# Optimization experiments

Measured on AMD Instinct MI355X. Metric: run time of the kernel, lower is better.

The kernel has to match this reference:

```python
import jax, jax.numpy as jnp
import numpy as np

B = 64      # num graphs
NPG = 800   # nodes per graph
N = B * NPG
EPG = 6400  # edges per graph (avg degree 8)
APG = 64    # feasible actions per graph
H = 4       # attention heads
C = 64      # hidden channels per head
OUT = 128   # out_channels


def _gat_params(key, fin, h, c, concat):
    k1, k2, k3 = jax.random.split(key, 3)
    s = 1.0 / np.sqrt(fin)
    W = jax.random.uniform(k1, (fin, h * c), jnp.float32, -s, s)
    a_src = jax.random.uniform(k2, (h, c), jnp.float32, -s, s)
    a_dst = jax.random.uniform(k3, (h, c), jnp.float32, -s, s)
    b = jnp.zeros((h * c if concat else c,), jnp.float32)
    return W, a_src, a_dst, b


def _lin_params(key, fin, fout):
    k1, k2 = jax.random.split(key)
    s = 1.0 / np.sqrt(fin)
    W = jax.random.uniform(k1, (fin, fout), jnp.float32, -s, s)
    b = jax.random.uniform(k2, (fout,), jnp.float32, -s, s)
    return W, b


def setup_inputs() -> dict:
    key = jax.random.key(0)
    ks = list(jax.random.split(key, 24))
    x = jax.random.normal(ks[0], (N, 5), jnp.float32)
    offs = jnp.arange(B, dtype=jnp.int32) * NPG
    src = jax.random.randint(ks[1], (B, EPG), 0, NPG, jnp.int32) + offs[:, None]
    dst = jax.random.randint(ks[2], (B, EPG), 0, NPG, jnp.int32) + offs[:, None]
    edge_index = jnp.stack([src.reshape(-1), dst.reshape(-1)])
    batch = jnp.repeat(jnp.arange(B, dtype=jnp.int32), NPG)
    actions_idx = (jax.random.randint(ks[3], (B, APG, 2), 0, NPG, jnp.int32)
                   + offs[:, None, None]).reshape(-1, 2)
    tabu_label = (jax.random.uniform(ks[4], (B * APG, 1)) < 0.5).astype(jnp.float32)
    inp = dict(x=x, edge_index=edge_index, batch=batch,
               actions_idx=actions_idx, tabu_label=tabu_label)
    names = ['f1', 'f2', 'f3', 'b1', 'b2', 'b3']
    fins = [3, H * C, H * C, 3, H * C, H * C]
    hs = [H, H, 1, H, H, 1]
    cs = [C, C, OUT, C, C, OUT]
    concats = [True, True, False, True, True, False]
    for i, nm in enumerate(names):
        W, a_s, a_d, b = _gat_params(ks[5 + i], fins[i], hs[i], cs[i], concats[i])
        inp[nm + '_W'] = W; inp[nm + '_as'] = a_s; inp[nm + '_ad'] = a_d; inp[nm + '_b'] = b
    dims = [(8 * OUT + 1, 2 * OUT), (2 * OUT, 2 * OUT), (2 * OUT, 2 * OUT), (2 * OUT, 1)]
    for i, (fi, fo) in enumerate(dims):
        W, b = _lin_params(ks[12 + i], fi, fo)
        inp['p_W%d' % (i + 1)] = W; inp['p_b%d' % (i + 1)] = b
    return inp


def _gat(h, s, d, W, a_src, a_dst, bias, concat):
    # PyG GATConv: project, per-edge attention, softmax over target index, scatter-add
    n = h.shape[0]
    Hh, Cc = a_src.shape
    xp = (h @ W).reshape(n, Hh, Cc)                      # [N,H,C]
    al_s = (xp * a_src).sum(-1)                          # [N,H]
    al_d = (xp * a_dst).sum(-1)                          # [N,H]
    e = jax.nn.leaky_relu(al_s[s] + al_d[d], 0.2)        # [E,H]
    m = jax.ops.segment_max(e, d, num_segments=n)
    ex = jnp.exp(e - m[d])
    den = jax.ops.segment_sum(ex, d, num_segments=n)
    alpha = ex / (den[d] + 1e-16)
    out = jax.ops.segment_sum(xp[s] * alpha[..., None], d, num_segments=n)  # [N,H,C]
    out = out.reshape(n, Hh * Cc) if concat else out.mean(axis=1)
    return out + bias


def reference(x, edge_index, batch, actions_idx, tabu_label,
              f1_W, f1_as, f1_ad, f1_b, f2_W, f2_as, f2_ad, f2_b,
              f3_W, f3_as, f3_ad, f3_b, b1_W, b1_as, b1_ad, b1_b,
              b2_W, b2_as, b2_ad, b2_b, b3_W, b3_as, b3_ad, b3_b,
              p_W1, p_b1, p_W2, p_b2, p_W3, p_b3, p_W4, p_b4):
    n = x.shape[0]
    ar = jnp.arange(n, dtype=edge_index.dtype)
    ei = jnp.concatenate([edge_index, jnp.stack([ar, ar])], axis=1)  # add_self_loops
    src, dst = ei[0], ei[1]
    # forward branch (flow source_to_target)
    hf = x[:, jnp.array([0, 1, 3])]
    hf = jax.nn.elu(_gat(hf, src, dst, f1_W, f1_as, f1_ad, f1_b, True))
    hf = jax.nn.elu(_gat(hf, src, dst, f2_W, f2_as, f2_ad, f2_b, True))
    hf3 = _gat(hf, src, dst, f3_W, f3_as, f3_ad, f3_b, False)
    # backward branch (flow target_to_source == reversed edges)
    hb = x[:, jnp.array([0, 2, 4])]
    hb = jax.nn.elu(_gat(hb, dst, src, b1_W, b1_as, b1_ad, b1_b, True))
    hb = jax.nn.elu(_gat(hb, dst, src, b2_W, b2_as, b2_ad, b2_b, True))
    hb3 = _gat(hb, dst, src, b3_W, b3_as, b3_ad, b3_b, False)
    h_node = jnp.concatenate([hf3, hb3], axis=-1)        # [N, 2*OUT]
    counts = jax.ops.segment_sum(jnp.ones((n,), x.dtype), batch, num_segments=B)
    g_pool = jax.ops.segment_sum(h_node, batch, num_segments=B) / counts[:, None]
    node_h = jnp.concatenate([h_node, g_pool[batch]], axis=-1)  # [N, 4*OUT]
    action_h = jnp.concatenate([node_h[actions_idx[:, 0]],
                                node_h[actions_idx[:, 1]],
                                tabu_label], axis=-1)    # [A, 8*OUT+1]
    h = jnp.tanh(action_h @ p_W1 + p_b1)
    h = jnp.tanh(h @ p_W2 + p_b2)
    h = jnp.tanh(h @ p_W3 + p_b3)
    score = (h @ p_W4 + p_b4).reshape(B, APG)
    log_prob = jax.nn.log_softmax(score, axis=-1)        # [B, APG]
    entropy = -(jnp.exp(log_prob) * log_prob).sum(-1, keepdims=True)  # [B,1]
    return (log_prob, entropy)
```

## Files before the change

kernel.cpp:

```cpp
#include <hip/hip_runtime.h>
#include <hip/hip_bf16.h>
#include <math.h>

constexpr int NN  = 51200;
constexpr int EE  = 409600;
constexpr int BB  = 64;
constexpr int APG = 64;
constexpr int NPG = 800;
constexpr int SCAN_N = 2 * NN;
constexpr int NA = BB * APG;
constexpr int KF = 1056;

typedef __bf16 bf16x8 __attribute__((ext_vector_type(8)));
typedef float f32x4 __attribute__((ext_vector_type(4)));
typedef float f32x2 __attribute__((ext_vector_type(2)));
typedef __attribute__((address_space(1))) const void g_void;
typedef __attribute__((address_space(3))) void l_void;

__device__ __forceinline__ float leaky(float x) { return fmaxf(x, 0.2f * x); }
__device__ __forceinline__ float bflo(unsigned w) { return __uint_as_float(w << 16); }
__device__ __forceinline__ float bfhi(unsigned w) { return __uint_as_float(w & 0xffff0000u); }
__device__ __forceinline__ unsigned short f2b(float x) {
  __hip_bfloat16 h = __float2bfloat16(x);
  unsigned short u;
  __builtin_memcpy(&u, &h, 2);
  return u;
}
__device__ __forceinline__ unsigned pack2(float a, float b) {
  return (unsigned)f2b(a) | ((unsigned)f2b(b) << 16);
}

__global__ void count_kernel(const int* __restrict__ ei, int* cnt) {
  int e = blockIdx.x * blockDim.x + threadIdx.x;
  if (e >= EE) return;
  int s = ei[e], d = ei[EE + e];
  atomicAdd(&cnt[d], 1);
  atomicAdd(&cnt[NN + s], 1);
}

__global__ __launch_bounds__(256) void scan1_kernel(const int* __restrict__ cnt,
                                                    int* __restrict__ rp,
                                                    int* __restrict__ bsum) {
  __shared__ int wsum[4];
  int b = blockIdx.x, t = threadIdx.x;
  int base = b * 1024 + t * 4;
  int4 v = *(const int4*)(cnt + base);
  int s = v.x + v.y + v.z + v.w;
  int lane = t & 63, wv = t >> 6;
  int incl = s;
  for (int off = 1; off < 64; off <<= 1) {
    int u = __shfl_up(incl, off);
    if (lane >= off) incl += u;
  }
  if (lane == 63) wsum[wv] = incl;
  __syncthreads();
  int woff = 0;
  for (int i = 0; i < wv; i++) woff += wsum[i];
  int excl = woff + incl - s;
  rp[base] = excl;
  rp[base + 1] = excl + v.x;
  rp[base + 2] = excl + v.x + v.y;
  rp[base + 3] = excl + v.x + v.y + v.z;
  if (t == 255) bsum[b] = woff + incl;
}

__global__ void scan2_kernel(const int* __restrict__ bsum, int* __restrict__ boff,
                             int* __restrict__ rp) {
  __shared__ int w0;
  int t = threadIdx.x;
  int v = (t < 100) ? bsum[t] : 0;
  int lane = t & 63;
  int incl = v;
  for (int off = 1; off < 64; off <<= 1) {
    int u = __shfl_up(incl, off);
    if (lane >= off) incl += u;
  }
  if (t == 63) w0 = incl;
  __syncthreads();
  int excl = incl - v + ((t >= 64) ? w0 : 0);
  if (t < 100) boff[t] = excl;
  if (t == 99) rp[SCAN_N] = excl + v;
}

__global__ __launch_bounds__(256) void scan3_kernel(int* __restrict__ rp,
                                                    const int* __restrict__ boff) {
  int b = blockIdx.x;
  int off = boff[b];
  int i = b * 1024 + threadIdx.x * 4;
  int4 v = *(int4*)(rp + i);
  v.x += off; v.y += off; v.z += off; v.w += off;
  *(int4*)(rp + i) = v;
}

__global__ void fill_kernel(const int* __restrict__ ei, const int* __restrict__ rp,
                            int* pos, int* __restrict__ col) {
  int e = blockIdx.x * blockDim.x + threadIdx.x;
  if (e >= EE) return;
  int s = ei[e], d = ei[EE + e];
  int p = atomicAdd(&pos[d], 1);
  col[rp[d] + p] = s;
  int q = atomicAdd(&pos[NN + s], 1);
  col[rp[NN + s] + q] = d;
}

__global__ __launch_bounds__(256) void precomp_kernel(const float* __restrict__ Wf,
                                                      const float* __restrict__ Wb,
                                                      const float* __restrict__ asf,
                                                      const float* __restrict__ adf,
                                                      const float* __restrict__ asb,
                                                      const float* __restrict__ adb,
                                                      float* __restrict__ wa) {
  int wave = (blockIdx.x * blockDim.x + threadIdx.x) >> 6;
  int lane = threadIdx.x & 63;
  if (wave >= 48) return;
  int dir = wave / 24, sd = (wave / 12) % 2, h = (wave / 3) % 4, c = wave % 3;
  const float* W = dir ? Wb : Wf;
  const float* a = dir ? (sd ? adb : asb) : (sd ? adf : asf);
  float v = W[c * 256 + h * 64 + lane] * a[h * 64 + lane];
  for (int off = 1; off < 64; off <<= 1) v += __shfl_xor(v, off);
  if (lane == 0) wa[wave] = v;
}

__global__ __launch_bounds__(256) void lin1_kernel(const float* __restrict__ x,
                                                   const float* __restrict__ Wf,
                                                   const float* __restrict__ Wb,
                                                   const float* __restrict__ wa,
                                                   __hip_bfloat16* __restrict__ out,
                                                   float* __restrict__ al_s,
                                                   float* __restrict__ al_d) {
  int idx = blockIdx.x * 256 + threadIdx.x;
  int n = idx >> 5, grp = idx & 31;
  int dir = (n >= NN) ? 1 : 0;
  int node = dir ? n - NN : n;
  const float* W = dir ? Wb : Wf;
  int c1 = dir ? 2 : 1, c2 = dir ? 4 : 3;
  float f0 = x[node * 5], f1 = x[node * 5 + c1], f2 = x[node * 5 + c2];
  int j0 = grp * 8;
  float v[8];
#pragma unroll
  for (int j = 0; j < 8; j++)
    v[j] = f0 * W[j0 + j] + f1 * W[256 + j0 + j] + f2 * W[512 + j0 + j];
  uint4 u;
  u.x = pack2(v[0], v[1]);
  u.y = pack2(v[2], v[3]);
  u.z = pack2(v[4], v[5]);
  u.w = pack2(v[6], v[7]);
  *(uint4*)(out + (size_t)n * 256 + j0) = u;
  if (grp < 4) {
    const float* ws = wa + dir * 24 + grp * 3;
    const float* wd = wa + dir * 24 + 12 + grp * 3;
    al_s[n * 4 + grp] = f0 * ws[0] + f1 * ws[1] + f2 * ws[2];
    al_d[n * 4 + grp] = f0 * wd[0] + f1 * wd[1] + f2 * wd[2];
  }
}

__device__ __forceinline__ f32x2 unpk(unsigned w) {
  f32x2 v;
  v.x = bflo(w);
  v.y = bfhi(w);
  return v;
}

template <int HH, int CC, int OUT_SPLIT>
__global__ __launch_bounds__(256) void spmm_kernel(const __hip_bfloat16* __restrict__ xp,
                                                   const float* __restrict__ als,
                                                   const float* __restrict__ ald,
                                                   const int* __restrict__ rp,
                                                   const int* __restrict__ col,
                                                   const float* __restrict__ biasf,
                                                   const float* __restrict__ biasb,
                                                   __hip_bfloat16* __restrict__ out_bf,
                                                   int do_elu) {
  constexpr int HC = HH * CC;
  constexpr int RDW = HC / 2;
  constexpr int DL = RDW / 32;
  constexpr int NWQ = (HH == 4) ? 8 : 2;
  int b = blockIdx.x;
  int xcd = b & 7;
  int bq = b >> 3;
  int dreg = xcd * 12800;
  int t = threadIdx.x;
  int wv = t >> 6, lane = t & 63;
  int sub = lane & 31, halfsel = lane >> 5;
  int lbase = lane & 32;
  int off_row = (dreg >= NN) ? NN : 0;
  const float* bias = (dreg >= NN) ? biasb : biasf;
  int hch = (HH == 4) ? (sub >> 3) : 0;
  int hat = (HH == 4) ? (sub & 3) : 0;
  const unsigned* xw = (const unsigned*)xp;
  float bv[2 * DL];
#pragma unroll
  for (int j = 0; j < 2 * DL; j++) bv[j] = bias[sub * 2 * DL + j];

#pragma unroll 1
  for (int it = 0; it < 4; ++it) {
    int d = dreg + it * 3200 + bq * 8 + wv * 2 + halfsel;
    int beg = rp[d];
    int deg = rp[d + 1] - beg;
    int degmax = max(deg, __shfl_xor(deg, 32));
    degmax = __builtin_amdgcn_readfirstlane(degmax);

    float ald_d = ald[(size_t)d * HH + hat];
    float als_d = als[(size_t)d * HH + hat];
    float selfw = __expf(leaky(als_d + ald_d));

    int e0 = (sub < deg) ? sub : (deg - 1);
    e0 = (e0 < 0) ? 0 : e0;
    int cA = col[beg + e0];
    cA = (((unsigned)cA < (unsigned)NN) ? cA : 0) + off_row;
    int cB = off_row;
    if (degmax > 32) {
      int e1 = (32 + sub < deg) ? (32 + sub) : (deg - 1);
      e1 = (e1 < 0) ? 0 : e1;
      cB = col[beg + e1];
      cB = (((unsigned)cB < (unsigned)NN) ? cB : 0) + off_row;
    }

    float wq[NWQ];
    float den = 0.f;
    if constexpr (HH == 4) {
#pragma unroll
      for (int g = 0; g < 8; ++g) {
        float w = 0.f;
        if (g * 8 < degmax) {
          int e = g * 8 + (sub >> 2);
          int s = __shfl((g < 4) ? cA : cB, lbase + (g & 3) * 8 + (sub >> 2));
          if (e < deg) w = __expf(leaky(als[(size_t)s * 4 + hat] + ald_d));
        }
        wq[g] = w;
        den += w;
      }
      for (int e = 64; e < degmax; ++e) {
        if (e < deg) {
          int s = col[beg + e];
          s = (((unsigned)s < (unsigned)NN) ? s : 0) + off_row;
          den += __expf(leaky(als[(size_t)s * 4 + hat] + ald_d));
        }
      }
      den += __shfl_xor(den, 4);
      den += __shfl_xor(den, 8);
      den += __shfl_xor(den, 16);
    } else {
#pragma unroll
      for (int g = 0; g < 2; ++g) {
        float w = 0.f;
        if (g * 32 < degmax) {
          int e = g * 32 + sub;
          int s = g ? cB : cA;
          if (e < deg) w = __expf(leaky(als[s] + ald_d));
        }
        wq[g] = w;
        den += w;
      }
      for (int e = 64; e < degmax; ++e) {
        if (e < deg) {
          int s = col[beg + e];
          s = (((unsigned)s < (unsigned)NN) ? s : 0) + off_row;
          den += __expf(leaky(als[s] + ald_d));
        }
      }
      den += __shfl_xor(den, 1);
      den += __shfl_xor(den, 2);
      den += __shfl_xor(den, 4);
      den += __shfl_xor(den, 8);
      den += __shfl_xor(den, 16);
    }
    float inv = 1.f / (den + selfw + 1e-16f);
#pragma unroll
    for (int g = 0; g < NWQ; ++g) wq[g] *= inv;
    float aself = selfw * inv;
    if constexpr (HH == 4) aself = __shfl(aself, lbase + (sub >> 3));

    f32x2 acc[DL];
    {
      const unsigned* sp = xw + (size_t)d * RDW + sub * DL;
      if constexpr (DL == 4) {
        uint4 sw = *(const uint4*)sp;
        acc[0] = aself * unpk(sw.x);
        acc[1] = aself * unpk(sw.y);
        acc[2] = aself * unpk(sw.z);
        acc[3] = aself * unpk(sw.w);
      } else {
        uint2 sw = *(const uint2*)sp;
        acc[0] = aself * unpk(sw.x);
        acc[1] = aself * unpk(sw.y);
      }
    }
#pragma unroll
    for (int c = 0; c < 8; ++c) {
      if (c * 8 < degmax) {
        uint4 w8[8];
#pragma unroll
        for (int k = 0; k < 8; ++k) {
          int s = __shfl((c < 4) ? cA : cB, lbase + (c & 3) * 8 + k);
          const unsigned* p = xw + (size_t)s * RDW + sub * DL;
          if constexpr (DL == 4) {
            w8[k] = *(const uint4*)p;
          } else {
            uint2 v2 = *(const uint2*)p;
            w8[k].x = v2.x;
            w8[k].y = v2.y;
          }
        }
#pragma unroll
        for (int k = 0; k < 8; ++k) {
          float a;
          if constexpr (HH == 4) a = __shfl(wq[c], lbase + k * 4 + hch);
          else a = __shfl(wq[c >> 2], lbase + (c & 3) * 8 + k);
          acc[0] += a * unpk(w8[k].x);
          acc[1] += a * unpk(w8[k].y);
          if constexpr (DL == 4) {
            acc[2] += a * unpk(w8[k].z);
            acc[3] += a * unpk(w8[k].w);
          }
        }
      }
    }
    if (degmax > 64) {
      float invc = inv, aldc = ald_d;
      if constexpr (HH == 4) {
        invc = __shfl(inv, lbase + (sub >> 3));
        aldc = __shfl(ald_d, lbase + (sub >> 3));
      }
      for (int e = 64; e < degmax; ++e) {
        if (e < deg) {
          int s = col[beg + e];
          s = (((unsigned)s < (unsigned)NN) ? s : 0) + off_row;
          float a = __expf(leaky(als[(size_t)s * HH + hch] + aldc)) * invc;
          const unsigned* p = xw + (size_t)s * RDW + sub * DL;
          acc[0] += a * unpk(p[0]);
          acc[1] += a * unpk(p[1]);
          if constexpr (DL == 4) {
            acc[2] += a * unpk(p[2]);
            acc[3] += a * unpk(p[3]);
          }
        }
      }
    }

    float v[2 * DL];
#pragma unroll
    for (int j = 0; j < DL; j++) {
      v[2 * j] = acc[j].x + bv[2 * j];
      v[2 * j + 1] = acc[j].y + bv[2 * j + 1];
    }
    if (do_elu) {
#pragma unroll
      for (int j = 0; j < 2 * DL; j++) v[j] = v[j] > 0.f ? v[j] : (__expf(v[j]) - 1.f);
    }
    if constexpr (OUT_SPLIT) {
      int nd = (d < NN) ? d : d - NN;
      int oo = (d < NN) ? 0 : 64;
      uint2 u;
      u.x = pack2(v[0], v[1]);
      u.y = pack2(v[2], v[3]);
      *(uint2*)((unsigned*)out_bf + (size_t)nd * 128 + oo + sub * 2) = u;
    } else {
      uint4 u;
      u.x = pack2(v[0], v[1]);
      u.y = pack2(v[2], v[3]);
      u.z = pack2(v[4], v[5]);
      u.w = pack2(v[6], v[7]);
      *(uint4*)((unsigned*)out_bf + (size_t)d * RDW + sub * DL) = u;
    }
  }
}

__global__ void castW2_kernel(const float* __restrict__ W0, const float* __restrict__ W1,
                              __hip_bfloat16* __restrict__ Wt0,
                              __hip_bfloat16* __restrict__ Wt1,
                              int K, int N, int Kp) {
  int idx = blockIdx.x * 256 + threadIdx.x;
  int tot = N * Kp;
  if (idx >= 2 * tot) return;
  const float* W = (idx < tot) ? W0 : W1;
  __hip_bfloat16* Wt = (idx < tot) ? Wt0 : Wt1;
  int i = (idx < tot) ? idx : idx - tot;
  int n = i / Kp, k = i % Kp;
  Wt[i] = (k < K) ? __float2bfloat16(W[(size_t)k * N + n]) : __float2bfloat16(0.f);
}

__global__ void castW1_kernel(const float* __restrict__ W, __hip_bfloat16* __restrict__ Wt,
                              int K, int N, int Kp) {
  int idx = blockIdx.x * 256 + threadIdx.x;
  if (idx >= N * Kp) return;
  int n = idx / Kp, k = idx % Kp;
  Wt[idx] = (k < K) ? __float2bfloat16(W[(size_t)k * N + n]) : __float2bfloat16(0.f);
}

template <int EPI, int ALH, int ALCC>
__global__ __launch_bounds__(256) void gemm_mfma(const __hip_bfloat16* __restrict__ A,
                                                 const __hip_bfloat16* __restrict__ Bt0,
                                                 const __hip_bfloat16* __restrict__ Bt1,
                                                 __hip_bfloat16* __restrict__ Cb,
                                                 const float* __restrict__ bias0,
                                                 const float* __restrict__ bias1,
                                                 const float* __restrict__ asv0,
                                                 const float* __restrict__ asv1,
                                                 const float* __restrict__ adv0,
                                                 const float* __restrict__ adv1,
                                                 float* __restrict__ al_s,
                                                 float* __restrict__ al_d,
                                                 int M, int N, int K, int Mhalf) {
  __shared__ __align__(16) __hip_bfloat16 As[128 * 32];
  __shared__ __align__(16) __hip_bfloat16 Bs[128 * 32];
  int t = threadIdx.x;
  int wave = t >> 6, lane = t & 63;
  int wm = (wave >> 1) * 64, wn = (wave & 1) * 64;
  int bm = blockIdx.y * 128, bn = blockIdx.x * 128;
  bool second = bm >= Mhalf;
  const __hip_bfloat16* Bt = second ? Bt1 : Bt0;
  const float* bias = second ? bias1 : bias0;
  const float* asv = second ? asv1 : asv0;
  const float* adv = second ? adv1 : adv0;

  int r0 = t >> 2, c0 = (t & 3) * 8;
  const __hip_bfloat16* Ag0 = A + (size_t)(bm + r0) * K + c0;
  const __hip_bfloat16* Ag1 = A + (size_t)(bm + r0 + 64) * K + c0;
  const __hip_bfloat16* Bg0 = Bt + (size_t)(bn + r0) * K + c0;
  const __hip_bfloat16* Bg1 = Bt + (size_t)(bn + r0 + 64) * K + c0;
  __hip_bfloat16* Asp0 = As + t * 8;
  __hip_bfloat16* Asp1 = As + 64 * 8 * 4 + t * 8;
  __hip_bfloat16* Bsp0 = Bs + t * 8;
  __hip_bfloat16* Bsp1 = Bs + 64 * 8 * 4 + t * 8;

  f32x4 acc[4][4];
#pragma unroll
  for (int i = 0; i < 4; i++)
#pragma unroll
    for (int j = 0; j < 4; j++) acc[i][j] = (f32x4)(0.f);

  int frag_off = (lane & 15) * 32 + (lane >> 4) * 8;
  const __hip_bfloat16* Ab = As + wm * 32 + frag_off;
  const __hip_bfloat16* Bb = Bs + wn * 32 + frag_off;

  for (int k0 = 0; k0 < K; k0 += 32) {
    __syncthreads();
    __builtin_amdgcn_global_load_lds((g_void*)(Ag0 + k0), (l_void*)Asp0, 16, 0, 0);
    __builtin_amdgcn_global_load_lds((g_void*)(Ag1 + k0), (l_void*)Asp1, 16, 0, 0);
    __builtin_amdgcn_global_load_lds((g_void*)(Bg0 + k0), (l_void*)Bsp0, 16, 0, 0);
    __builtin_amdgcn_global_load_lds((g_void*)(Bg1 + k0), (l_void*)Bsp1, 16, 0, 0);
    __syncthreads();
    bf16x8 af[4], bfr[4];
#pragma unroll
    for (int i = 0; i < 4; i++) af[i] = *(const bf16x8*)(Ab + i * 16 * 32);
#pragma unroll
    for (int j = 0; j < 4; j++) bfr[j] = *(const bf16x8*)(Bb + j * 16 * 32);
#pragma unroll
    for (int i = 0; i < 4; i++)
#pragma unroll
      for (int j = 0; j < 4; j++)
        acc[i][j] = __builtin_amdgcn_mfma_f32_16x16x32_bf16(af[i], bfr[j], acc[i][j], 0, 0, 0);
  }

  int cr = (lane >> 4) * 4, cc = lane & 15;

  if constexpr (ALH > 0) {
    int head = (bn + wn) / ALCC;
    float as_c[4], ad_c[4];
#pragma unroll
    for (int j = 0; j < 4; j++) {
      int colx = bn + wn + j * 16 + cc;
      as_c[j] = asv[colx];
      ad_c[j] = adv[colx];
    }
#pragma unroll
    for (int i = 0; i < 4; i++)
#pragma unroll
      for (int r = 0; r < 4; r++) {
        float ps = 0.f, pd = 0.f;
#pragma unroll
        for (int j = 0; j < 4; j++) {
          ps += acc[i][j][r] * as_c[j];
          pd += acc[i][j][r] * ad_c[j];
        }
        ps += __shfl_xor(ps, 1); pd += __shfl_xor(pd, 1);
        ps += __shfl_xor(ps, 2); pd += __shfl_xor(pd, 2);
        ps += __shfl_xor(ps, 4); pd += __shfl_xor(pd, 4);
        ps += __shfl_xor(ps, 8); pd += __shfl_xor(pd, 8);
        if ((lane & 15) == 0) {
          int row = bm + wm + i * 16 + cr + r;
          if (ALCC > 64) {
            atomicAdd(&al_s[row * ALH + head], ps);
            atomicAdd(&al_d[row * ALH + head], pd);
          } else {
            al_s[row * ALH + head] = ps;
            al_d[row * ALH + head] = pd;
          }
        }
      }
  }

#pragma unroll
  for (int i = 0; i < 4; i++)
#pragma unroll
    for (int j = 0; j < 4; j++) {
      int colx = bn + wn + j * 16 + cc;
      float bs = (EPI == 2) ? bias[colx] : 0.f;
#pragma unroll
      for (int r = 0; r < 4; r++) {
        float v = acc[i][j][r];
        if (EPI == 2) v = tanhf(v + bs);
        Cb[(size_t)(bm + wm + i * 16 + cr + r) * N + colx] = __float2bfloat16(v);
      }
    }
}

__global__ void pool1_kernel(const __hip_bfloat16* __restrict__ h_node,
                             float* __restrict__ part) {
  int g = blockIdx.y, c = blockIdx.x, t = threadIdx.x;
  const unsigned* base = (const unsigned*)h_node + ((size_t)g * NPG + c * 100) * 128 + t;
  f32x2 s = (f32x2)(0.f);
  for (int i = 0; i < 100; i++) s += unpk(base[(size_t)i * 128]);
  part[(size_t)(g * 8 + c) * 256 + 2 * t] = s.x;
  part[(size_t)(g * 8 + c) * 256 + 2 * t + 1] = s.y;
}

__global__ void pool2_kernel(const float* __restrict__ part, float* __restrict__ g_pool) {
  int g = blockIdx.x, t = threadIdx.x;
  float s = 0.f;
  for (int c = 0; c < 8; c++) s += part[(size_t)(g * 8 + c) * 256 + t];
  g_pool[g * 256 + t] = s * (1.f / NPG);
}

__global__ __launch_bounds__(256) void buildfeat_kernel(const __hip_bfloat16* __restrict__ h_node,
                                                        const float* __restrict__ g_pool,
                                                        const int* __restrict__ actions,
                                                        const float* __restrict__ tabu,
                                                        const int* __restrict__ batch,
                                                        __hip_bfloat16* __restrict__ feat) {
  int a = (blockIdx.x * blockDim.x + threadIdx.x) >> 6;
  int lane = threadIdx.x & 63;
  if (a >= NA) return;
  int n0 = actions[a * 2], n1 = actions[a * 2 + 1];
  int g = batch[n0];
  ushort4 v0 = *(const ushort4*)(h_node + (size_t)n0 * 256 + lane * 4);
  float4 vg = *(const float4*)(g_pool + (size_t)g * 256 + lane * 4);
  ushort4 v1 = *(const ushort4*)(h_node + (size_t)n1 * 256 + lane * 4);
  __hip_bfloat16* fr = feat + (size_t)a * KF;
  ushort4 ug = make_ushort4(f2b(vg.x), f2b(vg.y), f2b(vg.z), f2b(vg.w));
  *(ushort4*)(fr + lane * 4) = v0;
  *(ushort4*)(fr + 256 + lane * 4) = ug;
  *(ushort4*)(fr + 512 + lane * 4) = v1;
  *(ushort4*)(fr + 768 + lane * 4) = ug;
  if (lane < 8) {
    float t0 = (lane == 0) ? tabu[a] : 0.f;
    ushort4 u = make_ushort4(f2b(t0), 0, 0, 0);
    *(ushort4*)(fr + 1024 + lane * 4) = u;
  }
}

__global__ __launch_bounds__(256) void head_kernel(const __hip_bfloat16* __restrict__ y,
                                                   const float* __restrict__ W4,
                                                   const float* __restrict__ b4,
                                                   float* __restrict__ out) {
  __shared__ float sc[64];
  int g = blockIdx.x;
  int t = threadIdx.x;
  int a = t >> 2, sub = t & 3;
  int aid = g * 64 + a;
  const unsigned* row = (const unsigned*)(y + (size_t)aid * 256) + sub * 32;
  const float* w = W4 + sub * 64;
  float s = 0.f;
#pragma unroll
  for (int q = 0; q < 32; q++) {
    s += bflo(row[q]) * w[2 * q] + bfhi(row[q]) * w[2 * q + 1];
  }
  s += __shfl_xor(s, 1);
  s += __shfl_xor(s, 2);
  if (sub == 0) sc[a] = s + b4[0];
  __syncthreads();
  if (t < 64) {
    float v = sc[t];
    float m = v;
    for (int off = 1; off < 64; off <<= 1) m = fmaxf(m, __shfl_xor(m, off));
    float ex = expf(v - m);
    float sum = ex;
    for (int off = 1; off < 64; off <<= 1) sum += __shfl_xor(sum, off);
    float lp = v - m - logf(sum);
    out[g * 64 + t] = lp;
    float pe = (ex / sum) * lp;
    for (int off = 1; off < 64; off <<= 1) pe += __shfl_xor(pe, off);
    if (t == 0) out[BB * APG + g] = -pe;
  }
}

extern "C" void kernel_launch(void* const* d_in, const int* in_sizes, int n_in,
                              void* d_out, int out_size, void* d_ws, size_t ws_size,
                              hipStream_t stream) {
  const float* x = (const float*)d_in[0];
  const int* ei = (const int*)d_in[1];
  const int* batch = (const int*)d_in[2];
  const int* actions = (const int*)d_in[3];
  const float* tabu = (const float*)d_in[4];
  const float* fW[3] = {(const float*)d_in[5], (const float*)d_in[9], (const float*)d_in[13]};
  const float* fas[3] = {(const float*)d_in[6], (const float*)d_in[10], (const float*)d_in[14]};
  const float* fad[3] = {(const float*)d_in[7], (const float*)d_in[11], (const float*)d_in[15]};
  const float* fb[3] = {(const float*)d_in[8], (const float*)d_in[12], (const float*)d_in[16]};
  const float* bW[3] = {(const float*)d_in[17], (const float*)d_in[21], (const float*)d_in[25]};
  const float* bas[3] = {(const float*)d_in[18], (const float*)d_in[22], (const float*)d_in[26]};
  const float* bad[3] = {(const float*)d_in[19], (const float*)d_in[23], (const float*)d_in[27]};
  const float* bb[3] = {(const float*)d_in[20], (const float*)d_in[24], (const float*)d_in[28]};
  const float* pW1 = (const float*)d_in[29];
  const float* pb1 = (const float*)d_in[30];
  const float* pW2 = (const float*)d_in[31];
  const float* pb2 = (const float*)d_in[32];
  const float* pW3 = (const float*)d_in[33];
  const float* pb3 = (const float*)d_in[34];
  const float* pW4 = (const float*)d_in[35];
  const float* pb4 = (const float*)d_in[36];
  float* out = (float*)d_out;

  char* ws = (char*)d_ws;
  size_t o = 0;
  auto alloc = [&](size_t bytes) -> void* {
    o = (o + 255) & ~(size_t)255;
    void* p = ws + o;
    o += bytes;
    return p;
  };
  int* cnt = (int*)alloc((size_t)4 * NN * 4);
  int* rp = (int*)alloc((size_t)(SCAN_N + 1) * 4);
  int* col = (int*)alloc(((size_t)2 * EE + 64) * 4);
  int* bsum = (int*)alloc(128 * 4);
  int* boff = (int*)alloc(128 * 4);
  float* al_s = (float*)alloc((size_t)SCAN_N * 4 * 4);
  float* al_d = (float*)alloc((size_t)SCAN_N * 4 * 4);
  __hip_bfloat16* xp = (__hip_bfloat16*)alloc((size_t)SCAN_N * 256 * 2);
  __hip_bfloat16* bufA = (__hip_bfloat16*)alloc((size_t)SCAN_N * 256 * 2);
  __hip_bfloat16* h_node = (__hip_bfloat16*)alloc((size_t)NN * 256 * 2);
  __hip_bfloat16* wt0 = (__hip_bfloat16*)alloc((size_t)256 * KF * 2);
  __hip_bfloat16* wt1 = (__hip_bfloat16*)alloc((size_t)256 * KF * 2);
  float* part = (float*)alloc((size_t)BB * 8 * 256 * 4);
  float* g_pool = (float*)alloc((size_t)BB * 256 * 4);
  float* wa = (float*)alloc(64 * 4);
  __hip_bfloat16* feat = xp;
  __hip_bfloat16* y1 = feat + (size_t)NA * KF;
  __hip_bfloat16* y2 = y1 + (size_t)NA * 256;

  hipMemsetAsync(cnt, 0, (size_t)4 * NN * 4, stream);
  count_kernel<<<(EE + 255) / 256, 256, 0, stream>>>(ei, cnt);
  scan1_kernel<<<SCAN_N / 1024, 256, 0, stream>>>(cnt, rp, bsum);
  scan2_kernel<<<1, 128, 0, stream>>>(bsum, boff, rp);
  scan3_kernel<<<SCAN_N / 1024, 256, 0, stream>>>(rp, boff);
  fill_kernel<<<(EE + 255) / 256, 256, 0, stream>>>(ei, rp, cnt + 2 * NN, col);

  const int nwb = 3200;

  precomp_kernel<<<12, 256, 0, stream>>>(fW[0], bW[0], fas[0], fad[0], bas[0], bad[0], wa);
  lin1_kernel<<<SCAN_N * 32 / 256, 256, 0, stream>>>(x, fW[0], bW[0], wa, xp, al_s, al_d);
  spmm_kernel<4, 64, 0><<<nwb, 256, 0, stream>>>(xp, al_s, al_d, rp, col,
                                                 fb[0], bb[0], bufA, 1);
  castW2_kernel<<<(2 * 256 * 256 + 255) / 256, 256, 0, stream>>>(fW[1], bW[1], wt0, wt1,
                                                                 256, 256, 256);
  gemm_mfma<1, 4, 64><<<dim3(2, SCAN_N / 128), 256, 0, stream>>>(
      bufA, wt0, wt1, xp, nullptr, nullptr, fas[1], bas[1], fad[1], bad[1],
      al_s, al_d, SCAN_N, 256, 256, NN);
  spmm_kernel<4, 64, 0><<<nwb, 256, 0, stream>>>(xp, al_s, al_d, rp, col,
                                                 fb[1], bb[1], bufA, 1);
  castW2_kernel<<<(2 * 128 * 256 + 255) / 256, 256, 0, stream>>>(fW[2], bW[2], wt0, wt1,
                                                                 256, 128, 256);
  hipMemsetAsync(al_s, 0, (size_t)2 * SCAN_N * 4, stream);
  gemm_mfma<1, 1, 128><<<dim3(1, SCAN_N / 128), 256, 0, stream>>>(
      bufA, wt0, wt1, xp, nullptr, nullptr, fas[2], bas[2], fad[2], bad[2],
      al_s, al_d, SCAN_N, 128, 256, NN);
  spmm_kernel<1, 128, 1><<<nwb, 256, 0, stream>>>(xp, al_s, al_d, rp, col,
                                                  fb[2], bb[2], h_node, 0);

  pool1_kernel<<<dim3(8, BB), 128, 0, stream>>>(h_node, part);
  pool2_kernel<<<BB, 256, 0, stream>>>(part, g_pool);

  buildfeat_kernel<<<NA / 4, 256, 0, stream>>>(h_node, g_pool, actions, tabu, batch, feat);
  castW1_kernel<<<(256 * KF + 255) / 256, 256, 0, stream>>>(pW1, wt0, 1025, 256, KF);
  gemm_mfma<2, 0, 64><<<dim3(2, NA / 128), 256, 0, stream>>>(
      feat, wt0, wt0, y1, pb1, pb1, nullptr, nullptr, nullptr, nullptr,
      nullptr, nullptr, NA, 256, KF, 1 << 30);
  castW2_kernel<<<(2 * 256 * 256 + 255) / 256, 256, 0, stream>>>(pW2, pW3, wt0, wt1,
                                                                 256, 256, 256);
  gemm_mfma<2, 0, 64><<<dim3(2, NA / 128), 256, 0, stream>>>(
      y1, wt0, wt0, y2, pb2, pb2, nullptr, nullptr, nullptr, nullptr,
      nullptr, nullptr, NA, 256, 256, 1 << 30);
  gemm_mfma<2, 0, 64><<<dim3(2, NA / 128), 256, 0, stream>>>(
      y2, wt1, wt1, y1, pb3, pb3, nullptr, nullptr, nullptr, nullptr,
      nullptr, nullptr, NA, 256, 256, 1 << 30);
  head_kernel<<<BB, 256, 0, stream>>>(y1, pW4, pb4, out);
}
```

Baseline: 511.7 us.

## Fuse softmax denominator into SpMM aggregation loop and coarsen lin1 grid

The GAT SpMM kernel no longer makes a separate pass to compute and normalize edge weights. Unnormalized exp weights are computed inside the gather loop, the denominator is accumulated alongside, and normalization plus the self-loop term are applied once at the end. This removes a pass over neighbor attention scores and the wq register array, and the >64-degree tail now does a single pass instead of two. Separately, lin1 processes 8 chunks per block with a smaller grid to cut block launch overhead.

```diff
diff --git a/kernel.cpp b/kernel.cpp
--- a/kernel.cpp
+++ b/kernel.cpp
@@ -128,29 +128,32 @@
                                                    __hip_bfloat16* __restrict__ out,
                                                    float* __restrict__ al_s,
                                                    float* __restrict__ al_d) {
-  int idx = blockIdx.x * 256 + threadIdx.x;
-  int n = idx >> 5, grp = idx & 31;
-  int dir = (n >= NN) ? 1 : 0;
-  int node = dir ? n - NN : n;
-  const float* W = dir ? Wb : Wf;
-  int c1 = dir ? 2 : 1, c2 = dir ? 4 : 3;
-  float f0 = x[node * 5], f1 = x[node * 5 + c1], f2 = x[node * 5 + c2];
-  int j0 = grp * 8;
-  float v[8];
-#pragma unroll
-  for (int j = 0; j < 8; j++)
-    v[j] = f0 * W[j0 + j] + f1 * W[256 + j0 + j] + f2 * W[512 + j0 + j];
-  uint4 u;
-  u.x = pack2(v[0], v[1]);
-  u.y = pack2(v[2], v[3]);
-  u.z = pack2(v[4], v[5]);
-  u.w = pack2(v[6], v[7]);
-  *(uint4*)(out + (size_t)n * 256 + j0) = u;
-  if (grp < 4) {
-    const float* ws = wa + dir * 24 + grp * 3;
-    const float* wd = wa + dir * 24 + 12 + grp * 3;
-    al_s[n * 4 + grp] = f0 * ws[0] + f1 * ws[1] + f2 * ws[2];
-    al_d[n * 4 + grp] = f0 * wd[0] + f1 * wd[1] + f2 * wd[2];
+#pragma unroll 1
+  for (int itq = 0; itq < 8; ++itq) {
+    int idx = blockIdx.x * 2048 + itq * 256 + threadIdx.x;
+    int n = idx >> 5, grp = idx & 31;
+    int dir = (n >= NN) ? 1 : 0;
+    int node = dir ? n - NN : n;
+    const float* W = dir ? Wb : Wf;
+    int c1 = dir ? 2 : 1, c2 = dir ? 4 : 3;
+    float f0 = x[node * 5], f1 = x[node * 5 + c1], f2 = x[node * 5 + c2];
+    int j0 = grp * 8;
+    float v[8];
+#pragma unroll
+    for (int j = 0; j < 8; j++)
+      v[j] = f0 * W[j0 + j] + f1 * W[256 + j0 + j] + f2 * W[512 + j0 + j];
+    uint4 u;
+    u.x = pack2(v[0], v[1]);
+    u.y = pack2(v[2], v[3]);
+    u.z = pack2(v[4], v[5]);
+    u.w = pack2(v[6], v[7]);
+    *(uint4*)(out + (size_t)n * 256 + j0) = u;
+    if (grp < 4) {
+      const float* ws = wa + dir * 24 + grp * 3;
+      const float* wd = wa + dir * 24 + 12 + grp * 3;
+      al_s[n * 4 + grp] = f0 * ws[0] + f1 * ws[1] + f2 * ws[2];
+      al_d[n * 4 + grp] = f0 * wd[0] + f1 * wd[1] + f2 * wd[2];
+    }
   }
 }
 
@@ -174,7 +177,6 @@
   constexpr int HC = HH * CC;
   constexpr int RDW = HC / 2;
   constexpr int DL = RDW / 32;
-  constexpr int NWQ = (HH == 4) ? 8 : 2;
   int b = blockIdx.x;
   int xcd = b & 7;
   int bq = b >> 3;
@@ -187,6 +189,7 @@
   const float* bias = (dreg >= NN) ? biasb : biasf;
   int hch = (HH == 4) ? (sub >> 3) : 0;
   int hat = (HH == 4) ? (sub & 3) : 0;
+  int eg  = (HH == 4) ? (sub >> 2) : (sub & 7);
   const unsigned* xw = (const unsigned*)xp;
   float bv[2 * DL];
 #pragma unroll
@@ -201,8 +204,7 @@
     degmax = __builtin_amdgcn_readfirstlane(degmax);
 
     float ald_d = ald[(size_t)d * HH + hat];
-    float als_d = als[(size_t)d * HH + hat];
-    float selfw = __expf(leaky(als_d + ald_d));
+    float selfw = __expf(leaky(als[(size_t)d * HH + hat] + ald_d));
 
     int e0 = (sub < deg) ? sub : (deg - 1);
     e0 = (e0 < 0) ? 0 : e0;
@@ -216,79 +218,28 @@
       cB = (((unsigned)cB < (unsigned)NN) ? cB : 0) + off_row;
     }
 
-    float wq[NWQ];
-    float den = 0.f;
-    if constexpr (HH == 4) {
-#pragma unroll
-      for (int g = 0; g < 8; ++g) {
-        float w = 0.f;
-        if (g * 8 < degmax) {
-          int e = g * 8 + (sub >> 2);
-          int s = __shfl((g < 4) ? cA : cB, lbase + (g & 3) * 8 + (sub >> 2));
-          if (e < deg) w = __expf(leaky(als[(size_t)s * 4 + hat] + ald_d));
-        }
-        wq[g] = w;
-        den += w;
-      }
-      for (int e = 64; e < degmax; ++e) {
-        if (e < deg) {
-          int s = col[beg + e];
-          s = (((unsigned)s < (unsigned)NN) ? s : 0) + off_row;
-          den += __expf(leaky(als[(size_t)s * 4 + hat] + ald_d));
-        }
-      }
-      den += __shfl_xor(den, 4);
-      den += __shfl_xor(den, 8);
-      den += __shfl_xor(den, 16);
-    } else {
-#pragma unroll
-      for (int g = 0; g < 2; ++g) {
-        float w = 0.f;
-        if (g * 32 < degmax) {
-          int e = g * 32 + sub;
-          int s = g ? cB : cA;
-          if (e < deg) w = __expf(leaky(als[s] + ald_d));
-        }
-        wq[g] = w;
-        den += w;
-      }
-      for (int e = 64; e < degmax; ++e) {
-        if (e < deg) {
-          int s = col[beg + e];
-          s = (((unsigned)s < (unsigned)NN) ? s : 0) + off_row;
-          den += __expf(leaky(als[s] + ald_d));
-        }
-      }
-      den += __shfl_xor(den, 1);
-      den += __shfl_xor(den, 2);
-      den += __shfl_xor(den, 4);
-      den += __shfl_xor(den, 8);
-      den += __shfl_xor(den, 16);
-    }
-    float inv = 1.f / (den + selfw + 1e-16f);
-#pragma unroll
-    for (int g = 0; g < NWQ; ++g) wq[g] *= inv;
-    float aself = selfw * inv;
-    if constexpr (HH == 4) aself = __shfl(aself, lbase + (sub >> 3));
-
-    f32x2 acc[DL];
+    unsigned swa[4] = {0u, 0u, 0u, 0u};
     {
       const unsigned* sp = xw + (size_t)d * RDW + sub * DL;
       if constexpr (DL == 4) {
-        uint4 sw = *(const uint4*)sp;
-        acc[0] = aself * unpk(sw.x);
-        acc[1] = aself * unpk(sw.y);
-        acc[2] = aself * unpk(sw.z);
-        acc[3] = aself * unpk(sw.w);
+        uint4 v4 = *(const uint4*)sp;
+        swa[0] = v4.x; swa[1] = v4.y; swa[2] = v4.z; swa[3] = v4.w;
       } else {
-        uint2 sw = *(const uint2*)sp;
-        acc[0] = aself * unpk(sw.x);
-        acc[1] = aself * unpk(sw.y);
+        uint2 v2 = *(const uint2*)sp;
+        swa[0] = v2.x; swa[1] = v2.y;
       }
     }
+
+    f32x2 acc[DL];
+#pragma unroll
+    for (int j = 0; j < DL; j++) acc[j] = (f32x2)(0.f);
+    float den = 0.f;
+
 #pragma unroll
     for (int c = 0; c < 8; ++c) {
       if (c * 8 < degmax) {
+        int sg = __shfl((c < 4) ? cA : cB, lbase + (c & 3) * 8 + eg);
+        float alsv = als[(size_t)sg * HH + hat];
         uint4 w8[8];
 #pragma unroll
         for (int k = 0; k < 8; ++k) {
@@ -302,11 +253,13 @@
             w8[k].y = v2.y;
           }
         }
+        float w = 0.f;
+        if (c * 8 + eg < deg) w = __expf(leaky(alsv + ald_d));
+        if constexpr (HH == 4) den += w;
+        else den += (sub < 8) ? w : 0.f;
 #pragma unroll
         for (int k = 0; k < 8; ++k) {
-          float a;
-          if constexpr (HH == 4) a = __shfl(wq[c], lbase + k * 4 + hch);
-          else a = __shfl(wq[c >> 2], lbase + (c & 3) * 8 + k);
+          float a = __shfl(w, lbase + ((HH == 4) ? (k * 4 + hch) : k));
           acc[0] += a * unpk(w8[k].x);
           acc[1] += a * unpk(w8[k].y);
           if constexpr (DL == 4) {
@@ -316,33 +269,50 @@
         }
       }
     }
-    if (degmax > 64) {
-      float invc = inv, aldc = ald_d;
-      if constexpr (HH == 4) {
-        invc = __shfl(inv, lbase + (sub >> 3));
-        aldc = __shfl(ald_d, lbase + (sub >> 3));
-      }
-      for (int e = 64; e < degmax; ++e) {
-        if (e < deg) {
-          int s = col[beg + e];
-          s = (((unsigned)s < (unsigned)NN) ? s : 0) + off_row;
-          float a = __expf(leaky(als[(size_t)s * HH + hch] + aldc)) * invc;
-          const unsigned* p = xw + (size_t)s * RDW + sub * DL;
-          acc[0] += a * unpk(p[0]);
-          acc[1] += a * unpk(p[1]);
-          if constexpr (DL == 4) {
-            acc[2] += a * unpk(p[2]);
-            acc[3] += a * unpk(p[3]);
-          }
+    for (int e = 64; e < degmax; ++e) {
+      if (e < deg) {
+        int s = col[beg + e];
+        s = (((unsigned)s < (unsigned)NN) ? s : 0) + off_row;
+        float w = __expf(leaky(als[(size_t)s * HH + hat] + ald_d));
+        if constexpr (HH == 4) den += (sub < 4) ? w : 0.f;
+        else den += (sub == 0) ? w : 0.f;
+        float a;
+        if constexpr (HH == 4) a = __shfl(w, lbase + hch);
+        else a = w;
+        const unsigned* p = xw + (size_t)s * RDW + sub * DL;
+        acc[0] += a * unpk(p[0]);
+        acc[1] += a * unpk(p[1]);
+        if constexpr (DL == 4) {
+          acc[2] += a * unpk(p[2]);
+          acc[3] += a * unpk(p[3]);
         }
       }
     }
 
+    if constexpr (HH == 4) {
+      den += __shfl_xor(den, 4);
+      den += __shfl_xor(den, 8);
+      den += __shfl_xor(den, 16);
+    } else {
+      den += __shfl_xor(den, 1);
+      den += __shfl_xor(den, 2);
+      den += __shfl_xor(den, 4);
+      den += __shfl_xor(den, 8);
+      den += __shfl_xor(den, 16);
+    }
+    float inv = 1.f / (den + selfw + 1e-16f);
+    float invc = inv, selfc = selfw;
+    if constexpr (HH == 4) {
+      invc = __shfl(inv, lbase + hch);
+      selfc = __shfl(selfw, lbase + hch);
+    }
+
     float v[2 * DL];
 #pragma unroll
     for (int j = 0; j < DL; j++) {
-      v[2 * j] = acc[j].x + bv[2 * j];
-      v[2 * j + 1] = acc[j].y + bv[2 * j + 1];
+      f32x2 r = acc[j] + selfc * unpk(swa[j]);
+      v[2 * j] = r.x * invc + bv[2 * j];
+      v[2 * j + 1] = r.y * invc + bv[2 * j + 1];
     }
     if (do_elu) {
 #pragma unroll
@@ -648,7 +618,7 @@
   const int nwb = 3200;
 
   precomp_kernel<<<12, 256, 0, stream>>>(fW[0], bW[0], fas[0], fad[0], bas[0], bad[0], wa);
-  lin1_kernel<<<SCAN_N * 32 / 256, 256, 0, stream>>>(x, fW[0], bW[0], wa, xp, al_s, al_d);
+  lin1_kernel<<<1600, 256, 0, stream>>>(x, fW[0], bW[0], wa, xp, al_s, al_d);
   spmm_kernel<4, 64, 0><<<nwb, 256, 0, stream>>>(xp, al_s, al_d, rp, col,
                                                  fb[0], bb[0], bufA, 1);
   castW2_kernel<<<(2 * 256 * 256 + 255) / 256, 256, 0, stream>>>(fW[1], bW[1], wt0, wt1,
```

Result: faster. 493.7 us (-3.5%).
